# Performance work log

Hardware: AMD Instinct MI355X
Metric: run time of the kernel (lower is better)

## Reference

```python
import jax, jax.numpy as jnp
import numpy as np

N = 100000
E = 3200000
F_IN, F_HID, F_OUT = 512, 16, 40


def gcn_conv(x, src, dst, W, b, n):
    # x: [N, Fin]; src/dst: [E_full] (self-loops included); W: [Fin, Fout]
    h = x @ W  # transform first (PyG GCNConv), [N, Fout]
    deg = jax.ops.segment_sum(jnp.ones_like(dst, dtype=h.dtype), dst, num_segments=n)
    dinv = jnp.where(deg > 0, jax.lax.rsqrt(deg), 0.0)  # D^{-1/2}
    norm = dinv[src] * dinv[dst]  # [E_full]
    msg = h[src] * norm[:, None]  # gather + scale
    out = jax.ops.segment_sum(msg, dst, num_segments=n)  # scatter-add
    return out + b


def setup_inputs() -> dict:
    key = jax.random.key(0)
    k1, k2, k3, k4, k5, k6 = jax.random.split(key, 6)
    x = jax.random.normal(k1, (N, F_IN), dtype=jnp.float32)
    edge_index = jax.random.randint(k2, (2, E), 0, N, dtype=jnp.int64)
    # glorot-ish scaled weights
    W1 = jax.random.normal(k3, (F_IN, F_HID), dtype=jnp.float32) * (1.0 / np.sqrt(F_IN))
    b1 = jnp.zeros((F_HID,), dtype=jnp.float32)
    W2 = jax.random.normal(k4, (F_HID, F_OUT), dtype=jnp.float32) * (1.0 / np.sqrt(F_HID))
    b2 = jnp.zeros((F_OUT,), dtype=jnp.float32)
    return {"x": x, "edge_index": edge_index, "W1": W1, "b1": b1, "W2": W2, "b2": b2}


def reference(x, edge_index, W1, b1, W2, b2):
    n = x.shape[0]
    loops = jnp.arange(n, dtype=edge_index.dtype)
    src = jnp.concatenate([edge_index[0], loops])  # add self-loops (PyG default)
    dst = jnp.concatenate([edge_index[1], loops])
    h = jax.nn.relu(gcn_conv(x, src, dst, W1, b1, n))
    h = gcn_conv(h, src, dst, W2, b2, n)
    return jax.nn.log_softmax(h, axis=1)
```

## Files before the change

kernel.cpp:

```cpp
#include <hip/hip_runtime.h>

#define FIN 512
#define FHID 16
#define FOUT 40
#define NBH 256
#define HWORDS_MAX 32768
#define BSH 9
#define NBKT_MAX 256

typedef __attribute__((ext_vector_type(8))) short bf16x8;
typedef __attribute__((ext_vector_type(4))) float f32x4;

#define ENC_S 32.0f
#define ENC_SI 0.03125f
#define ENC_B 8.0f

__device__ __forceinline__ unsigned long long enc4(float a, float b, float c, float d) {
    unsigned r0 = (unsigned)fmaf(a, ENC_S, 256.5f);
    unsigned r1 = (unsigned)fmaf(b, ENC_S, 256.5f);
    unsigned r2 = (unsigned)fmaf(c, ENC_S, 256.5f);
    unsigned r3 = (unsigned)fmaf(d, ENC_S, 256.5f);
    return (unsigned long long)r0 | ((unsigned long long)r1 << 16) |
           ((unsigned long long)r2 << 32) | ((unsigned long long)r3 << 48);
}

__device__ __forceinline__ unsigned bfpack2(float a, float b) {
    unsigned ua = __float_as_uint(a);
    unsigned ub = __float_as_uint(b);
    unsigned ra = (ua + 0x7fffu + ((ua >> 16) & 1u)) >> 16;
    unsigned rb = (ub + 0x7fffu + ((ub >> 16) & 1u)) & 0xffff0000u;
    return ra | rb;
}

__device__ __forceinline__ short bf1(float a) {
    unsigned ua = __float_as_uint(a);
    return (short)((ua + 0x7fffu + ((ua >> 16) & 1u)) >> 16);
}


__global__ __launch_bounds__(256) void k_hist(const int* __restrict__ dst,
                                              unsigned* __restrict__ histg,
                                              unsigned* __restrict__ bucketcnt,
                                              int E, int words, int nbkt) {
    __shared__ unsigned hist[HWORDS_MAX];
    int t = threadIdx.x;
    for (int i = t; i < words; i += 256) hist[i] = 0;
    __syncthreads();

    int chunk = (E + NBH - 1) / NBH;
    int beg = blockIdx.x * chunk;
    int end = beg + chunk; if (end > E) end = E;
    for (int i = beg + t; i < end; i += 256) {
        int d = dst[i];
        atomicAdd(&hist[d >> 2], 1u << ((d & 3) * 8));
    }
    __syncthreads();

    unsigned* outp = histg + (size_t)blockIdx.x * words;
    for (int i = t; i < words; i += 256) outp[i] = hist[i];

    if (t < NBKT_MAX) {
        unsigned s = 0;
        if (t < nbkt) {
            int w0 = t << (BSH - 2);
            int w1 = w0 + (1 << (BSH - 2)); if (w1 > words) w1 = words;
            for (int w = w0; w < w1; ++w) {
                unsigned v = hist[w];
                s += (v & 0xFFu) + ((v >> 8) & 0xFFu) + ((v >> 16) & 0xFFu) + ((v >> 24) & 0xFFu);
            }
        }
        bucketcnt[blockIdx.x * NBKT_MAX + t] = s;
    }
}


__global__ __launch_bounds__(256) void k_merge(const unsigned* __restrict__ histg,
                                               int words, int* __restrict__ cnt,
                                               float* __restrict__ dinv, int n) {
    int wd = blockIdx.x * 256 + threadIdx.x;
    if (wd >= words) return;
    unsigned s0 = 0, s1 = 0, s2 = 0, s3 = 0;
    const unsigned* p = histg + wd;
#pragma unroll 8
    for (int b = 0; b < NBH; ++b) {
        unsigned v = p[(size_t)b * words];
        s0 += v & 0xFFu;
        s1 += (v >> 8) & 0xFFu;
        s2 += (v >> 16) & 0xFFu;
        s3 += (v >> 24) & 0xFFu;
    }
    int nd = wd * 4;
    unsigned c[4] = {s0, s1, s2, s3};
#pragma unroll
    for (int j = 0; j < 4; ++j) {
        if (nd + j < n) {
            cnt[nd + j] = (int)c[j];
            dinv[nd + j] = rsqrtf((float)(c[j] + 1));
        }
    }
}


__global__ __launch_bounds__(256) void k_scanoff(const unsigned* __restrict__ bucketcnt,
                                                 unsigned* __restrict__ blockoff,
                                                 unsigned* __restrict__ bucketsum) {
    __shared__ unsigned part[256];
    int k = blockIdx.x, b = threadIdx.x;
    unsigned v = bucketcnt[b * NBKT_MAX + k];
    part[b] = v;
    __syncthreads();
    for (int off = 1; off < 256; off <<= 1) {
        unsigned u = (b >= off) ? part[b - off] : 0;
        __syncthreads();
        part[b] += u;
        __syncthreads();
    }
    blockoff[b * NBKT_MAX + k] = part[b] - v;
    if (b == 255) bucketsum[k] = part[255];
}


__global__ __launch_bounds__(256) void k_base(const unsigned* __restrict__ bucketsum,
                                              unsigned* __restrict__ bucketbase) {
    __shared__ unsigned part[256];
    int t = threadIdx.x;
    unsigned v = bucketsum[t];
    part[t] = v;
    __syncthreads();
    for (int off = 1; off < 256; off <<= 1) {
        unsigned u = (t >= off) ? part[t - off] : 0;
        __syncthreads();
        part[t] += u;
        __syncthreads();
    }
    bucketbase[t] = part[t] - v;
    if (t == 255) bucketbase[256] = part[255];
}


__global__ __launch_bounds__(256) void k_bfill(const int* __restrict__ src,
                                               const int* __restrict__ dst,
                                               const unsigned* __restrict__ bucketbase,
                                               const unsigned* __restrict__ blockoff,
                                               unsigned* __restrict__ sorted, int E) {
    __shared__ unsigned ldc[NBKT_MAX];
    __shared__ unsigned base_l[NBKT_MAX];
    int t = threadIdx.x, b = blockIdx.x;
    ldc[t] = 0;
    base_l[t] = bucketbase[t] + blockoff[b * NBKT_MAX + t];
    __syncthreads();

    int chunk = (E + NBH - 1) / NBH;
    int beg = b * chunk;
    int end = beg + chunk; if (end > E) end = E;
    for (int i = beg + t; i < end; i += 256) {
        int d = dst[i], s = src[i];
        int k = d >> BSH;
        unsigned r = atomicAdd(&ldc[k], 1u);
        sorted[base_l[k] + r] = ((unsigned)(d & ((1 << BSH) - 1)) << 17) | (unsigned)s;
    }
}


__global__ __launch_bounds__(256, 2) void k_gemm1(const float* __restrict__ x,
                                                  const float* __restrict__ W1,
                                                  const float* __restrict__ dinv,
                                                  unsigned long long* __restrict__ genc,
                                                  int n, int npanels) {
    __shared__ short xs[64 * 512];

    int t = threadIdx.x;
    int lane = t & 63;
    int wv = t >> 6;
    int kg = lane >> 4;
    int lcol = lane & 15;

    bf16x8 wf[16];
#pragma unroll
    for (int s = 0; s < 16; ++s) {
#pragma unroll
        for (int j = 0; j < 8; ++j)
            wf[s][j] = bf1(W1[(s * 32 + kg * 8 + j) * FHID + lcol]);
    }

    const size_t maxoff = (size_t)n * (FIN * 4) - 16;

    for (int pb = blockIdx.x; pb < npanels; pb += gridDim.x) {
        __syncthreads();

        size_t panelbyte = (size_t)pb * 131072;
#pragma unroll 1
        for (int b = 0; b < 4; ++b) {
            float4 v[8];
#pragma unroll
            for (int i = 0; i < 8; ++i) {
                size_t off = panelbyte + (size_t)(b * 8 + i) * 4096 + (size_t)t * 16;
                if (off > maxoff) off = maxoff;
                v[i] = *reinterpret_cast<const float4*>((const char*)x + off);
            }
#pragma unroll
            for (int i = 0; i < 8; ++i) {
                int elem = (b * 8 + i) * 1024 + t * 4;
                int row = elem >> 9;
                int kc = elem & 511;
                int kcs = kc ^ ((row & 7) << 3);
                uint2 w2;
                w2.x = bfpack2(v[i].x, v[i].y);
                w2.y = bfpack2(v[i].z, v[i].w);
                *reinterpret_cast<uint2*>(&xs[row * 512 + kcs]) = w2;
            }
        }
        __syncthreads();

        int lrow = wv * 16 + lcol;
        const short* ap = &xs[lrow * 512];
        f32x4 acc = {0.0f, 0.0f, 0.0f, 0.0f};
#pragma unroll
        for (int s = 0; s < 16; ++s) {
            int kc = s * 32 + kg * 8;
            bf16x8 a = *reinterpret_cast<const bf16x8*>(ap + (kc ^ ((lrow & 7) << 3)));
            acc = __builtin_amdgcn_mfma_f32_16x16x32_bf16(a, wf[s], acc, 0, 0, 0);
        }

        int panelrow = pb * 64 + wv * 16;
#pragma unroll
        for (int r = 0; r < 4; ++r) {
            int grow = panelrow + kg * 4 + r;
            float dv = (grow < n) ? dinv[grow] : 0.0f;
            float val = acc[r] * dv;
            float v1 = __shfl_xor(val, 1);
            float v2 = __shfl_xor(val, 2);
            float v3 = __shfl_xor(val, 3);
            if (grow < n && (lcol & 3) == 0)
                genc[(size_t)grow * 4 + (lcol >> 2)] = enc4(val, v1, v2, v3);
        }
    }
}


__global__ __launch_bounds__(256) void k_bagg(const unsigned* __restrict__ sorted,
                                              const unsigned* __restrict__ bucketbase,
                                              const unsigned long long* __restrict__ gin,
                                              unsigned long long* __restrict__ gout,
                                              int n) {
    __shared__ unsigned long long acc[512 * 4];
    int k = blockIdx.x, t = threadIdx.x;
    int node0 = k << BSH;
    int nlocal = n - node0; if (nlocal > 512) nlocal = 512;
    int lim = nlocal * 4;

    for (int i = t; i < 512 * 4; i += 256)
        acc[i] = (i < lim) ? gin[(size_t)node0 * 4 + i] : 0ULL;
    __syncthreads();

    int beg = (int)bucketbase[k], end = (int)bucketbase[k + 1];
    for (int i = beg + t; i < end; i += 256) {
        unsigned pr = sorted[i];
        int s = (int)(pr & 0x1FFFFu);
        int dl = (int)(pr >> 17);
        const ulonglong2* gp = reinterpret_cast<const ulonglong2*>(gin + (size_t)s * 4);
        ulonglong2 a = gp[0];
        ulonglong2 b = gp[1];
        unsigned long long* ap = &acc[dl * 4];
        atomicAdd(&ap[0], a.x);
        atomicAdd(&ap[1], a.y);
        atomicAdd(&ap[2], b.x);
        atomicAdd(&ap[3], b.y);
    }
    __syncthreads();

    for (int i = t; i < lim; i += 256)
        gout[(size_t)node0 * 4 + i] = acc[i];
}


__global__ void k_finish1(const unsigned long long* __restrict__ agg,
                          const int* __restrict__ cnt,
                          const float* __restrict__ dinv,
                          const float* __restrict__ b1,
                          unsigned long long* __restrict__ penc, int n) {
    int nd = blockIdx.x * blockDim.x + threadIdx.x;
    if (nd >= n) return;
    float dv = dinv[nd];
    float cb = (float)(cnt[nd] + 1) * ENC_B;
    const unsigned long long* ar = agg + (size_t)nd * 4;
    unsigned long long* pp = penc + (size_t)nd * 4;
#pragma unroll
    for (int j = 0; j < 4; ++j) {
        unsigned long long w = ar[j];
        float s0 = (float)(unsigned)(w & 0xFFFF) * ENC_SI - cb;
        float s1 = (float)(unsigned)((w >> 16) & 0xFFFF) * ENC_SI - cb;
        float s2 = (float)(unsigned)((w >> 32) & 0xFFFF) * ENC_SI - cb;
        float s3 = (float)(unsigned)((w >> 48) & 0xFFFF) * ENC_SI - cb;
        float r0 = fmaxf(fmaf(s0, dv, b1[4 * j + 0]), 0.0f) * dv;
        float r1 = fmaxf(fmaf(s1, dv, b1[4 * j + 1]), 0.0f) * dv;
        float r2 = fmaxf(fmaf(s2, dv, b1[4 * j + 2]), 0.0f) * dv;
        float r3 = fmaxf(fmaf(s3, dv, b1[4 * j + 3]), 0.0f) * dv;
        pp[j] = enc4(r0, r1, r2, r3);
    }
}


__global__ __launch_bounds__(256) void k_finish2(const unsigned long long* __restrict__ aggp,
                                                 const int* __restrict__ cnt,
                                                 const float* __restrict__ dinv,
                                                 const float* __restrict__ W2,
                                                 const float* __restrict__ b2,
                                                 float* __restrict__ out, int n) {
    __shared__ float Wl[FHID * FOUT];
    __shared__ float bl[FOUT];
    for (int i = threadIdx.x; i < FHID * FOUT; i += 256) Wl[i] = W2[i];
    if (threadIdx.x < FOUT) bl[threadIdx.x] = b2[threadIdx.x];
    __syncthreads();

    int nd = blockIdx.x * 256 + threadIdx.x;
    if (nd >= n) return;

    float dv = dinv[nd];
    float cb = (float)(cnt[nd] + 1) * ENC_B;
    float q[FHID];
    const unsigned long long* ap = aggp + (size_t)nd * 4;
#pragma unroll
    for (int j = 0; j < 4; ++j) {
        unsigned long long w = ap[j];
        q[4 * j + 0] = ((float)(unsigned)(w & 0xFFFF) * ENC_SI - cb) * dv;
        q[4 * j + 1] = ((float)(unsigned)((w >> 16) & 0xFFFF) * ENC_SI - cb) * dv;
        q[4 * j + 2] = ((float)(unsigned)((w >> 32) & 0xFFFF) * ENC_SI - cb) * dv;
        q[4 * j + 3] = ((float)(unsigned)((w >> 48) & 0xFFFF) * ENC_SI - cb) * dv;
    }

    float acc[FOUT];
#pragma unroll
    for (int o = 0; o < FOUT; ++o) acc[o] = bl[o];
#pragma unroll
    for (int kk = 0; kk < FHID; ++kk) {
        float qs = q[kk];
        const float* wrow = &Wl[kk * FOUT];
#pragma unroll
        for (int o = 0; o < FOUT; ++o) acc[o] = fmaf(qs, wrow[o], acc[o]);
    }

    float m = acc[0];
#pragma unroll
    for (int o = 1; o < FOUT; ++o) m = fmaxf(m, acc[o]);
    float ssum = 0.0f;
#pragma unroll
    for (int o = 0; o < FOUT; ++o) ssum += expf(acc[o] - m);
    float lse = m + logf(ssum);

    float4* op = reinterpret_cast<float4*>(out + (size_t)nd * FOUT);
#pragma unroll
    for (int tt = 0; tt < FOUT / 4; ++tt) {
        float4 v;
        v.x = acc[4 * tt + 0] - lse;
        v.y = acc[4 * tt + 1] - lse;
        v.z = acc[4 * tt + 2] - lse;
        v.w = acc[4 * tt + 3] - lse;
        op[tt] = v;
    }
}


extern "C" void kernel_launch(void* const* d_in, const int* in_sizes, int n_in,
                              void* d_out, int out_size, void* d_ws, size_t ws_size,
                              hipStream_t stream) {
    const float* x  = (const float*)d_in[0];
    const int*   ei = (const int*)d_in[1];
    const float* W1 = (const float*)d_in[2];
    const float* b1 = (const float*)d_in[3];
    const float* W2 = (const float*)d_in[4];
    const float* b2 = (const float*)d_in[5];

    const int fh = in_sizes[3];
    const int fi = in_sizes[2] / fh;
    const int n  = in_sizes[0] / fi;
    const int E  = in_sizes[1] / 2;
    (void)n_in; (void)out_size; (void)ws_size;

    const int* src = ei;
    const int* dst = ei + E;

    const int words = (n + 3) >> 2;
    const int nbkt = (n + (1 << BSH) - 1) >> BSH;

    char* w = (char*)d_ws;
    unsigned* histg     = (unsigned*)w;                 w += (size_t)NBH * words * 4;
    unsigned* bucketcnt = (unsigned*)w;                 w += (size_t)NBH * NBKT_MAX * 4;
    unsigned* blockoff  = (unsigned*)w;                 w += (size_t)NBH * NBKT_MAX * 4;
    unsigned* bucketsum = (unsigned*)w;                 w += (size_t)NBKT_MAX * 4;
    unsigned* bucketbase= (unsigned*)w;                 w += (size_t)(NBKT_MAX + 8) * 4;
    int*   cnt  = (int*)w;                              w += (size_t)n * 4;
    float* dinv = (float*)w;                            w += (size_t)n * 4;
    unsigned long long* genc = (unsigned long long*)w;  w += (size_t)n * 4 * 8;
    unsigned long long* agg  = (unsigned long long*)w;  w += (size_t)n * 4 * 8;
    unsigned long long* penc = (unsigned long long*)w;  w += (size_t)n * 4 * 8;
    unsigned long long* aggp = (unsigned long long*)w;  w += (size_t)n * 4 * 8;
    unsigned* sorted = (unsigned*)w;

    float* out = (float*)d_out;

    const int TB = 256;
    const int nb_n = (n + TB - 1) / TB;
    const int npanels = (n + 63) / 64;

    k_hist<<<NBH, TB, 0, stream>>>(dst, histg, bucketcnt, E, words, nbkt);
    k_merge<<<(words + TB - 1) / TB, TB, 0, stream>>>(histg, words, cnt, dinv, n);
    k_scanoff<<<NBKT_MAX, TB, 0, stream>>>(bucketcnt, blockoff, bucketsum);
    k_base<<<1, TB, 0, stream>>>(bucketsum, bucketbase);
    k_bfill<<<NBH, TB, 0, stream>>>(src, dst, bucketbase, blockoff, sorted, E);

    k_gemm1<<<512, TB, 0, stream>>>(x, W1, dinv, genc, n, npanels);

    k_bagg<<<nbkt, TB, 0, stream>>>(sorted, bucketbase, genc, agg, n);
    k_finish1<<<nb_n, TB, 0, stream>>>(agg, cnt, dinv, b1, penc, n);
    k_bagg<<<nbkt, TB, 0, stream>>>(sorted, bucketbase, penc, aggp, n);
    k_finish2<<<nb_n, TB, 0, stream>>>(aggp, cnt, dinv, W2, b2, out, n);
}
```

Before: 215.5 us.

## Fuse GCN finish stages into bucket aggregation and shrink buckets to 128 nodes

Merges the per-node finish kernels (bias, ReLU, re-encode for layer 1; dense W2, log-softmax for layer 2) into the bucketed shared-memory aggregation kernel through a LAYER template. This removes two launches and the round trip of the intermediate aggregate arrays through global memory. Buckets shrink from 512 to 128 nodes, giving 782 blocks instead of 196 for better occupancy, and the scans are widened to handle 1024 buckets. The gather loop is unrolled by four so more loads are in flight. The layer-2 epilogue uses only 128 of 256 threads per block, and the bucket count scans gain extra work.

```diff
diff --git a/kernel.cpp b/kernel.cpp
--- a/kernel.cpp
+++ b/kernel.cpp
@@ -5,8 +5,9 @@
 #define FOUT 40
 #define NBH 256
 #define HWORDS_MAX 32768
-#define BSH 9
-#define NBKT_MAX 256
+#define BSH 7
+#define NPB 128
+#define NBKT_MAX 1024
 
 typedef __attribute__((ext_vector_type(8))) short bf16x8;
 typedef __attribute__((ext_vector_type(4))) float f32x4;
@@ -59,17 +60,17 @@
     unsigned* outp = histg + (size_t)blockIdx.x * words;
     for (int i = t; i < words; i += 256) outp[i] = hist[i];
 
-    if (t < NBKT_MAX) {
+    for (int k = t; k < NBKT_MAX; k += 256) {
         unsigned s = 0;
-        if (t < nbkt) {
-            int w0 = t << (BSH - 2);
+        if (k < nbkt) {
+            int w0 = k << (BSH - 2);
             int w1 = w0 + (1 << (BSH - 2)); if (w1 > words) w1 = words;
             for (int w = w0; w < w1; ++w) {
                 unsigned v = hist[w];
                 s += (v & 0xFFu) + ((v >> 8) & 0xFFu) + ((v >> 16) & 0xFFu) + ((v >> 24) & 0xFFu);
             }
         }
-        bucketcnt[blockIdx.x * NBKT_MAX + t] = s;
+        bucketcnt[blockIdx.x * NBKT_MAX + k] = s;
     }
 }
 
@@ -124,8 +125,9 @@
                                               unsigned* __restrict__ bucketbase) {
     __shared__ unsigned part[256];
     int t = threadIdx.x;
-    unsigned v = bucketsum[t];
-    part[t] = v;
+    uint4 c4 = reinterpret_cast<const uint4*>(bucketsum)[t];
+    unsigned s = c4.x + c4.y + c4.z + c4.w;
+    part[t] = s;
     __syncthreads();
     for (int off = 1; off < 256; off <<= 1) {
         unsigned u = (t >= off) ? part[t - off] : 0;
@@ -133,8 +135,14 @@
         part[t] += u;
         __syncthreads();
     }
-    bucketbase[t] = part[t] - v;
-    if (t == 255) bucketbase[256] = part[255];
+    unsigned base = t ? part[t - 1] : 0;
+    uint4 o;
+    o.x = base;
+    o.y = o.x + c4.x;
+    o.z = o.y + c4.y;
+    o.w = o.z + c4.z;
+    reinterpret_cast<uint4*>(bucketbase)[t] = o;
+    if (t == 255) bucketbase[NBKT_MAX] = part[255];
 }
 
 
@@ -146,8 +154,10 @@
     __shared__ unsigned ldc[NBKT_MAX];
     __shared__ unsigned base_l[NBKT_MAX];
     int t = threadIdx.x, b = blockIdx.x;
-    ldc[t] = 0;
-    base_l[t] = bucketbase[t] + blockoff[b * NBKT_MAX + t];
+    for (int k = t; k < NBKT_MAX; k += 256) {
+        ldc[k] = 0;
+        base_l[k] = bucketbase[k] + blockoff[b * NBKT_MAX + k];
+    }
     __syncthreads();
 
     int chunk = (E + NBH - 1) / NBH;
@@ -157,7 +167,7 @@
         int d = dst[i], s = src[i];
         int k = d >> BSH;
         unsigned r = atomicAdd(&ldc[k], 1u);
-        sorted[base_l[k] + r] = ((unsigned)(d & ((1 << BSH) - 1)) << 17) | (unsigned)s;
+        sorted[base_l[k] + r] = ((unsigned)(d & (NPB - 1)) << 17) | (unsigned)s;
     }
 }
 
@@ -238,30 +248,63 @@
 }
 
 
+template <int LAYER>
 __global__ __launch_bounds__(256) void k_bagg(const unsigned* __restrict__ sorted,
                                               const unsigned* __restrict__ bucketbase,
                                               const unsigned long long* __restrict__ gin,
-                                              unsigned long long* __restrict__ gout,
-                                              int n) {
-    __shared__ unsigned long long acc[512 * 4];
+                                              const float* __restrict__ dinv,
+                                              const int* __restrict__ cnt,
+                                              const float* __restrict__ b1,
+                                              const float* __restrict__ W2,
+                                              const float* __restrict__ b2,
+                                              unsigned long long* __restrict__ penc,
+                                              float* __restrict__ out, int n) {
+    __shared__ unsigned long long acc[NPB * 4];
+    __shared__ float Wl[FHID * FOUT];
+    __shared__ float bl[FOUT];
+
     int k = blockIdx.x, t = threadIdx.x;
     int node0 = k << BSH;
-    int nlocal = n - node0; if (nlocal > 512) nlocal = 512;
+    int nlocal = n - node0; if (nlocal > NPB) nlocal = NPB;
     int lim = nlocal * 4;
 
-    for (int i = t; i < 512 * 4; i += 256)
+    for (int i = t; i < NPB * 4; i += 256)
         acc[i] = (i < lim) ? gin[(size_t)node0 * 4 + i] : 0ULL;
+    if (LAYER == 2) {
+        for (int i = t; i < FHID * FOUT; i += 256) Wl[i] = W2[i];
+        if (t < FOUT) bl[t] = b2[t];
+    }
     __syncthreads();
 
     int beg = (int)bucketbase[k], end = (int)bucketbase[k + 1];
-    for (int i = beg + t; i < end; i += 256) {
+    int i = beg + t;
+    for (; i + 256 * 3 < end; i += 256 * 4) {
+        unsigned pr[4];
+#pragma unroll
+        for (int j = 0; j < 4; ++j) pr[j] = sorted[i + 256 * j];
+        ulonglong2 a[4], b[4];
+#pragma unroll
+        for (int j = 0; j < 4; ++j) {
+            const ulonglong2* gp =
+                reinterpret_cast<const ulonglong2*>(gin + (size_t)(pr[j] & 0x1FFFFu) * 4);
+            a[j] = gp[0];
+            b[j] = gp[1];
+        }
+#pragma unroll
+        for (int j = 0; j < 4; ++j) {
+            unsigned long long* ap = &acc[(pr[j] >> 17) * 4];
+            atomicAdd(&ap[0], a[j].x);
+            atomicAdd(&ap[1], a[j].y);
+            atomicAdd(&ap[2], b[j].x);
+            atomicAdd(&ap[3], b[j].y);
+        }
+    }
+    for (; i < end; i += 256) {
         unsigned pr = sorted[i];
-        int s = (int)(pr & 0x1FFFFu);
-        int dl = (int)(pr >> 17);
-        const ulonglong2* gp = reinterpret_cast<const ulonglong2*>(gin + (size_t)s * 4);
-        ulonglong2 a = gp[0];
-        ulonglong2 b = gp[1];
-        unsigned long long* ap = &acc[dl * 4];
+        const ulonglong2* gp =
+            reinterpret_cast<const ulonglong2*>(gin + (size_t)(pr & 0x1FFFFu) * 4);
+        ulonglong2 a = gp[0], b = gp[1];
+        unsigned long long* ap = &acc[(pr >> 17) * 4];
         atomicAdd(&ap[0], a.x);
         atomicAdd(&ap[1], a.y);
         atomicAdd(&ap[2], b.x);
@@ -269,94 +312,65 @@
     }
     __syncthreads();
 
-    for (int i = t; i < lim; i += 256)
-        gout[(size_t)node0 * 4 + i] = acc[i];
-}
-
-
-__global__ void k_finish1(const unsigned long long* __restrict__ agg,
-                          const int* __restrict__ cnt,
-                          const float* __restrict__ dinv,
-                          const float* __restrict__ b1,
-                          unsigned long long* __restrict__ penc, int n) {
-    int nd = blockIdx.x * blockDim.x + threadIdx.x;
-    if (nd >= n) return;
-    float dv = dinv[nd];
-    float cb = (float)(cnt[nd] + 1) * ENC_B;
-    const unsigned long long* ar = agg + (size_t)nd * 4;
-    unsigned long long* pp = penc + (size_t)nd * 4;
-#pragma unroll
-    for (int j = 0; j < 4; ++j) {
-        unsigned long long w = ar[j];
-        float s0 = (float)(unsigned)(w & 0xFFFF) * ENC_SI - cb;
-        float s1 = (float)(unsigned)((w >> 16) & 0xFFFF) * ENC_SI - cb;
-        float s2 = (float)(unsigned)((w >> 32) & 0xFFFF) * ENC_SI - cb;
-        float s3 = (float)(unsigned)((w >> 48) & 0xFFFF) * ENC_SI - cb;
-        float r0 = fmaxf(fmaf(s0, dv, b1[4 * j + 0]), 0.0f) * dv;
-        float r1 = fmaxf(fmaf(s1, dv, b1[4 * j + 1]), 0.0f) * dv;
-        float r2 = fmaxf(fmaf(s2, dv, b1[4 * j + 2]), 0.0f) * dv;
-        float r3 = fmaxf(fmaf(s3, dv, b1[4 * j + 3]), 0.0f) * dv;
-        pp[j] = enc4(r0, r1, r2, r3);
-    }
-}
-
-
-__global__ __launch_bounds__(256) void k_finish2(const unsigned long long* __restrict__ aggp,
-                                                 const int* __restrict__ cnt,
-                                                 const float* __restrict__ dinv,
-                                                 const float* __restrict__ W2,
-                                                 const float* __restrict__ b2,
-                                                 float* __restrict__ out, int n) {
-    __shared__ float Wl[FHID * FOUT];
-    __shared__ float bl[FOUT];
-    for (int i = threadIdx.x; i < FHID * FOUT; i += 256) Wl[i] = W2[i];
-    if (threadIdx.x < FOUT) bl[threadIdx.x] = b2[threadIdx.x];
-    __syncthreads();
-
-    int nd = blockIdx.x * 256 + threadIdx.x;
-    if (nd >= n) return;
-
-    float dv = dinv[nd];
-    float cb = (float)(cnt[nd] + 1) * ENC_B;
-    float q[FHID];
-    const unsigned long long* ap = aggp + (size_t)nd * 4;
-#pragma unroll
-    for (int j = 0; j < 4; ++j) {
-        unsigned long long w = ap[j];
-        q[4 * j + 0] = ((float)(unsigned)(w & 0xFFFF) * ENC_SI - cb) * dv;
-        q[4 * j + 1] = ((float)(unsigned)((w >> 16) & 0xFFFF) * ENC_SI - cb) * dv;
-        q[4 * j + 2] = ((float)(unsigned)((w >> 32) & 0xFFFF) * ENC_SI - cb) * dv;
-        q[4 * j + 3] = ((float)(unsigned)((w >> 48) & 0xFFFF) * ENC_SI - cb) * dv;
-    }
-
-    float acc[FOUT];
-#pragma unroll
-    for (int o = 0; o < FOUT; ++o) acc[o] = bl[o];
-#pragma unroll
-    for (int kk = 0; kk < FHID; ++kk) {
-        float qs = q[kk];
-        const float* wrow = &Wl[kk * FOUT];
-#pragma unroll
-        for (int o = 0; o < FOUT; ++o) acc[o] = fmaf(qs, wrow[o], acc[o]);
-    }
-
-    float m = acc[0];
-#pragma unroll
-    for (int o = 1; o < FOUT; ++o) m = fmaxf(m, acc[o]);
-    float ssum = 0.0f;
-#pragma unroll
-    for (int o = 0; o < FOUT; ++o) ssum += expf(acc[o] - m);
-    float lse = m + logf(ssum);
-
-    float4* op = reinterpret_cast<float4*>(out + (size_t)nd * FOUT);
-#pragma unroll
-    for (int tt = 0; tt < FOUT / 4; ++tt) {
-        float4 v;
-        v.x = acc[4 * tt + 0] - lse;
-        v.y = acc[4 * tt + 1] - lse;
-        v.z = acc[4 * tt + 2] - lse;
-        v.w = acc[4 * tt + 3] - lse;
-        op[tt] = v;
+    if (LAYER == 1) {
+        for (int i2 = t; i2 < lim; i2 += 256) {
+            int nd = node0 + (i2 >> 2);
+            int j = i2 & 3;
+            float dv = dinv[nd];
+            float cb = (float)(cnt[nd] + 1) * ENC_B;
+            unsigned long long w = acc[i2];
+            float s0 = (float)(unsigned)(w & 0xFFFF) * ENC_SI - cb;
+            float s1 = (float)(unsigned)((w >> 16) & 0xFFFF) * ENC_SI - cb;
+            float s2 = (float)(unsigned)((w >> 32) & 0xFFFF) * ENC_SI - cb;
+            float s3 = (float)(unsigned)((w >> 48) & 0xFFFF) * ENC_SI - cb;
+            float r0 = fmaxf(fmaf(s0, dv, b1[4 * j + 0]), 0.0f) * dv;
+            float r1 = fmaxf(fmaf(s1, dv, b1[4 * j + 1]), 0.0f) * dv;
+            float r2 = fmaxf(fmaf(s2, dv, b1[4 * j + 2]), 0.0f) * dv;
+            float r3 = fmaxf(fmaf(s3, dv, b1[4 * j + 3]), 0.0f) * dv;
+            penc[(size_t)node0 * 4 + i2] = enc4(r0, r1, r2, r3);
+        }
+    } else {
+        if (t < nlocal) {
+            int nd = node0 + t;
+            float dv = dinv[nd];
+            float cb = (float)(cnt[nd] + 1) * ENC_B;
+            float q[FHID];
+#pragma unroll
+            for (int j = 0; j < 4; ++j) {
+                unsigned long long w = acc[t * 4 + j];
+                q[4 * j + 0] = ((float)(unsigned)(w & 0xFFFF) * ENC_SI - cb) * dv;
+                q[4 * j + 1] = ((float)(unsigned)((w >> 16) & 0xFFFF) * ENC_SI - cb) * dv;
+                q[4 * j + 2] = ((float)(unsigned)((w >> 32) & 0xFFFF) * ENC_SI - cb) * dv;
+                q[4 * j + 3] = ((float)(unsigned)((w >> 48) & 0xFFFF) * ENC_SI - cb) * dv;
+            }
+            float av[FOUT];
+#pragma unroll
+            for (int o = 0; o < FOUT; ++o) av[o] = bl[o];
+#pragma unroll
+            for (int kk = 0; kk < FHID; ++kk) {
+                float qs = q[kk];
+                const float* wrow = &Wl[kk * FOUT];
+#pragma unroll
+                for (int o = 0; o < FOUT; ++o) av[o] = fmaf(qs, wrow[o], av[o]);
+            }
+            float m = av[0];
+#pragma unroll
+            for (int o = 1; o < FOUT; ++o) m = fmaxf(m, av[o]);
+            float ssum = 0.0f;
+#pragma unroll
+            for (int o = 0; o < FOUT; ++o) ssum += expf(av[o] - m);
+            float lse = m + logf(ssum);
+            float4* op = reinterpret_cast<float4*>(out + (size_t)nd * FOUT);
+#pragma unroll
+            for (int tt = 0; tt < FOUT / 4; ++tt) {
+                float4 v;
+                v.x = av[4 * tt + 0] - lse;
+                v.y = av[4 * tt + 1] - lse;
+                v.z = av[4 * tt + 2] - lse;
+                v.w = av[4 * tt + 3] - lse;
+                op[tt] = v;
+            }
+        }
     }
 }
 
@@ -381,7 +395,7 @@
     const int* dst = ei + E;
 
     const int words = (n + 3) >> 2;
-    const int nbkt = (n + (1 << BSH) - 1) >> BSH;
+    const int nbkt = (n + NPB - 1) >> BSH;
 
     char* w = (char*)d_ws;
     unsigned* histg     = (unsigned*)w;                 w += (size_t)NBH * words * 4;
@@ -392,15 +406,12 @@
     int*   cnt  = (int*)w;                              w += (size_t)n * 4;
     float* dinv = (float*)w;                            w += (size_t)n * 4;
     unsigned long long* genc = (unsigned long long*)w;  w += (size_t)n * 4 * 8;
-    unsigned long long* agg  = (unsigned long long*)w;  w += (size_t)n * 4 * 8;
     unsigned long long* penc = (unsigned long long*)w;  w += (size_t)n * 4 * 8;
-    unsigned long long* aggp = (unsigned long long*)w;  w += (size_t)n * 4 * 8;
     unsigned* sorted = (unsigned*)w;
 
     float* out = (float*)d_out;
 
     const int TB = 256;
-    const int nb_n = (n + TB - 1) / TB;
     const int npanels = (n + 63) / 64;
 
     k_hist<<<NBH, TB, 0, stream>>>(dst, histg, bucketcnt, E, words, nbkt);
@@ -411,8 +422,8 @@
 
     k_gemm1<<<512, TB, 0, stream>>>(x, W1, dinv, genc, n, npanels);
 
-    k_bagg<<<nbkt, TB, 0, stream>>>(sorted, bucketbase, genc, agg, n);
-    k_finish1<<<nb_n, TB, 0, stream>>>(agg, cnt, dinv, b1, penc, n);
-    k_bagg<<<nbkt, TB, 0, stream>>>(sorted, bucketbase, penc, aggp, n);
-    k_finish2<<<nb_n, TB, 0, stream>>>(aggp, cnt, dinv, W2, b2, out, n);
-}
+    k_bagg<1><<<nbkt, TB, 0, stream>>>(sorted, bucketbase, genc, dinv, cnt, b1, W2, b2,
+                                       penc, out, n);
+    k_bagg<2><<<nbkt, TB, 0, stream>>>(sorted, bucketbase, penc, dinv, cnt, b1, W2, b2,
+                                       genc, out, n);
+}
```

Measured after the change: 203.8 us. 5.4% less time.
